# Performance work log

Hardware: AMD Instinct MI355X
Metric: run time of the kernel (lower is better)

Reference implementation:

```python
import jax, jax.numpy as jnp
import numpy as np

ALPHA = 0.2  # leaky relu slope

def setup_inputs() -> dict:
    key = jax.random.key(0)
    k1, k2, k3, k4 = jax.random.split(key, 4)
    b, n, din, dout = 8, 2048, 256, 128
    x = jax.random.normal(k1, (b, n, din), dtype=jnp.float32)
    adj = jax.random.randint(k2, (b, n, n), 0, 2, dtype=jnp.int32)
    # xavier-ish scaling for params
    W = jax.random.normal(k3, (dout, din), dtype=jnp.float32) * (1.414 * (2.0 / (din + dout)) ** 0.5)
    a = jax.random.normal(k4, (2 * dout,), dtype=jnp.float32) * (1.414 * (2.0 / (2 * dout + 1)) ** 0.5)
    return {"x": x, "adj": adj, "W": W, "a": a}

def reference(x, adj, W, a):
    # x: [b, n, din]; W: [dout, din]; a: [2*dout]
    wh = jnp.einsum('bnd,od->bno', x, W)           # [b, n, dout]
    dout = W.shape[0]
    a_src, a_dst = a[:dout], a[dout:]
    # e_ij = leaky_relu(a_src . wh_i + a_dst . wh_j)  (decomposed, avoids O(n^2 * 2d) concat)
    e = (wh @ a_src)[:, :, None] + (wh @ a_dst)[:, None, :]  # [b, n, n]
    e = jnp.where(e >= 0, e, ALPHA * e)
    e = jnp.where(adj != 0, e, -jnp.inf)
    attention = jax.nn.softmax(e, axis=2)          # [b, n, n]
    out = jnp.einsum('bij,bjo->bio', attention, wh)  # [b, n, dout]
    return jax.nn.relu(out)
```

## Files before the change

kernel.cpp:

```cpp
#include <hip/hip_runtime.h>
#include <hip/hip_bf16.h>
#include <stdint.h>

#define GAT_ALPHA 0.2f
#define LOG2E 1.4426950408889634f

typedef __attribute__((ext_vector_type(8))) __bf16 bf16x8;
typedef __attribute__((ext_vector_type(4))) float f32x4;

union B8 {
  bf16x8 b;
  unsigned short u[8];
  unsigned int w[4];
  int4 i4;
};

__device__ __forceinline__ unsigned int pk2bf(float lo, float hi) {
  union { __hip_bfloat162 h; unsigned int u; } cv;
  cv.h = __float22bfloat162_rn(make_float2(lo, hi));
  return cv.u;
}

__device__ __forceinline__ void dma16(const void* g, void* l) {
  __builtin_amdgcn_global_load_lds(
      (const __attribute__((address_space(1))) unsigned int*)g,
      (__attribute__((address_space(3))) unsigned int*)l, 16, 0, 0);
}

__global__ __launch_bounds__(256, 2) void gat_wh(
    const float* __restrict__ x, const float* __restrict__ W,
    const float* __restrict__ a, unsigned short* __restrict__ whTf,
    float* __restrict__ s_out, float* __restrict__ d_out) {
  __shared__ unsigned short WF[8][4][512];
  const int tid = threadIdx.x;
  const int wave = tid >> 6, lane = tid & 63;
  const int il = lane & 15, quad = lane >> 4;
  const int row0 = blockIdx.x * 64;
  const int i = row0 + wave * 16 + il;
  B8 av[8];
  {
    const float* xp = x + (size_t)i * 256 + quad * 8;
#pragma unroll
    for (int kc = 0; kc < 8; ++kc) {
      float4 lo = *(const float4*)(xp + kc * 32);
      float4 hi = *(const float4*)(xp + kc * 32 + 4);
      av[kc].w[0] = pk2bf(lo.x, lo.y);
      av[kc].w[1] = pk2bf(lo.z, lo.w);
      av[kc].w[2] = pk2bf(hi.x, hi.y);
      av[kc].w[3] = pk2bf(hi.z, hi.w);
    }
  }
  f32x4 acc[8];
#pragma unroll
  for (int nt = 0; nt < 8; ++nt) acc[nt] = (f32x4){0.f, 0.f, 0.f, 0.f};
#pragma unroll
  for (int h = 0; h < 2; ++h) {
    if (h) __syncthreads();
#pragma unroll
    for (int p = 0; p < 16; ++p) {
      const int f = p * 1024 + tid * 4;
      const int o = f >> 7, kk = f & 127;
      float4 v = *(const float4*)(W + o * 256 + h * 128 + kk);
      uint2 pk;
      pk.x = pk2bf(v.x, v.y);
      pk.y = pk2bf(v.z, v.w);
      *(uint2*)(&WF[o >> 4][kk >> 5][((o & 15) + (((kk & 31) >> 3) << 4)) * 8 + (kk & 7)]) = pk;
    }
    __syncthreads();
#pragma unroll
    for (int kl = 0; kl < 4; ++kl) {
      const int kc = h * 4 + kl;
#pragma unroll
      for (int nt = 0; nt < 8; ++nt) {
        B8 bv;
        bv.i4 = *(const int4*)(&WF[nt][kl][lane * 8]);
        acc[nt] = __builtin_amdgcn_mfma_f32_16x16x32_bf16(av[kc].b, bv.b, acc[nt], 0, 0, 0);
      }
    }
  }
  float asrc[8], adst[8];
#pragma unroll
  for (int nt = 0; nt < 8; ++nt) {
    asrc[nt] = a[nt * 16 + il];
    adst[nt] = a[128 + nt * 16 + il];
  }
  float sp[4], dp[4];
#pragma unroll
  for (int r = 0; r < 4; ++r) {
    float sv = 0.f, dv = 0.f;
#pragma unroll
    for (int nt = 0; nt < 8; ++nt) {
      sv += acc[nt][r] * asrc[nt];
      dv += acc[nt][r] * adst[nt];
    }
    sp[r] = sv; dp[r] = dv;
  }
#pragma unroll
  for (int off = 1; off <= 8; off <<= 1) {
#pragma unroll
    for (int r = 0; r < 4; ++r) {
      sp[r] += __shfl_xor(sp[r], off, 64);
      dp[r] += __shfl_xor(dp[r], off, 64);
    }
  }
  if (il == 0) {
#pragma unroll
    for (int r = 0; r < 4; ++r) {
      s_out[row0 + wave * 16 + quad * 4 + r] = sp[r];
      d_out[row0 + wave * 16 + quad * 4 + r] = dp[r];
    }
  }
  const int b = row0 >> 11;
  const int jc = ((row0 & 2047) >> 5) + (wave >> 1);
  const int kin = ((wave & 1) << 4) + (quad << 2);
  const int kq = kin >> 3, u0 = kin & 7;
#pragma unroll
  for (int nt = 0; nt < 8; ++nt) {
    uint2 pk;
    pk.x = pk2bf(acc[nt][0], acc[nt][1]);
    pk.y = pk2bf(acc[nt][2], acc[nt][3]);
    *(uint2*)(whTf + ((((size_t)(b * 64 + jc)) * 8 + nt) << 9) + ((il + (kq << 4)) << 3) + u0) = pk;
  }
}

#define ATTN_COMPUTE(Tval, CUR)                                                    \
  _Pragma("unroll") for (int c = 0; c < 2; ++c) {                                  \
    const int j0 = (2 * (Tval) + c) * 32;                                          \
    const unsigned int mq = (unsigned int)(mcur >> (32 * c + qo));                 \
    const float4 d0 = *(const float4*)(&dl[j0 + qo]);                              \
    const float4 d1 = *(const float4*)(&dl[j0 + qo + 4]);                          \
    const float dd[8] = {d0.x, d0.y, d0.z, d0.w, d1.x, d1.y, d1.z, d1.w};          \
    B8 af[8];                                                                      \
    _Pragma("unroll") for (int nt = 0; nt < 8; ++nt)                               \
        af[nt].i4 = *(const int4*)((const char*)&vbuf[CUR][c][nt][0] + lane * 16); \
    float pv[8];                                                                   \
    _Pragma("unroll") for (int u = 0; u < 8; ++u) {                                \
      float t0 = svL + dd[u];                                                      \
      float e2 = fmaxf(t0, GAT_ALPHA * t0);                                        \
      float p = __builtin_amdgcn_exp2f(e2);                                        \
      p = ((mq >> u) & 1u) ? p : 0.f;                                              \
      den += p;                                                                    \
      pv[u] = p;                                                                   \
    }                                                                              \
    B8 pf;                                                                         \
    pf.w[0] = pk2bf(pv[0], pv[1]);                                                 \
    pf.w[1] = pk2bf(pv[2], pv[3]);                                                 \
    pf.w[2] = pk2bf(pv[4], pv[5]);                                                 \
    pf.w[3] = pk2bf(pv[6], pv[7]);                                                 \
    _Pragma("unroll") for (int nt = 0; nt < 8; ++nt)                               \
      acc[nt] = __builtin_amdgcn_mfma_f32_16x16x32_bf16(af[nt].b, pf.b,            \
                                                        acc[nt], 0, 0, 0);         \
  }

#define ATTN_BALLOT(LVC)                                                           \
  {                                                                                \
    unsigned long long sel = __ballot(LVC[0] != 0);                                \
    _Pragma("unroll") for (int r = 1; r < 16; ++r) {                               \
      const unsigned long long mm = __ballot(LVC[r] != 0);                         \
      sel = (il == r) ? mm : sel;                                                  \
    }                                                                              \
    mcur = sel;                                                                    \
  }

#define ATTN_DMA(PAIR, NXT)                                                        \
  _Pragma("unroll") for (int h = 0; h < 2; ++h) {                                  \
    const int nt = wave * 2 + h;                                                   \
    dma16(whTb + (((size_t)(2 * (PAIR)) * 8 + nt) << 9) + (lane << 3),             \
          &vbuf[NXT][0][nt][0]);                                                   \
    dma16(whTb + (((size_t)(2 * (PAIR) + 1) * 8 + nt) << 9) + (lane << 3),         \
          &vbuf[NXT][1][nt][0]);                                                   \
  }

__global__ __launch_bounds__(256) void gat_attn(
    const int* __restrict__ adj, const unsigned short* __restrict__ whTf,
    const float* __restrict__ s, const float* __restrict__ dvec,
    float* __restrict__ out) {
  __shared__ unsigned short vbuf[2][2][8][512];
  __shared__ float dl[2048];
  const int tid = threadIdx.x;
  const int wave = tid >> 6;
  const int lane = tid & 63;
  const int il = lane & 15;
  const int quad = lane >> 4;
  const int qo = quad << 3;
  const int b = blockIdx.x & 7;
  const int tile = blockIdx.x >> 3;
  const int rbase = tile * 64;
  {
    const float* dsrc = dvec + ((size_t)b << 11);
#pragma unroll
    for (int it = 0; it < 2; ++it) {
      const int idx = it * 1024 + tid * 4;
      float4 v = *(const float4*)(dsrc + idx);
      v.x *= LOG2E; v.y *= LOG2E; v.z *= LOG2E; v.w *= LOG2E;
      *(float4*)(&dl[idx]) = v;
    }
  }
  const int* aro = adj + ((((size_t)b << 11) + rbase + wave * 16) << 11);
  int lv0[16], lvA[16], lvB[16];
#pragma unroll
  for (int r = 0; r < 16; ++r) lv0[r] = aro[(r << 11) + lane];
#pragma unroll
  for (int r = 0; r < 16; ++r) lvA[r] = aro[(r << 11) + 64 + lane];
  const unsigned short* whTb = whTf + (((size_t)b * 64) << 12);
  ATTN_DMA(0, 0);
  const int i = rbase + wave * 16 + il;
  const size_t browi = ((size_t)b << 11) + i;
  const float svL = s[browi] * LOG2E;
  f32x4 acc[8];
#pragma unroll
  for (int nt = 0; nt < 8; ++nt) acc[nt] = (f32x4){0.f, 0.f, 0.f, 0.f};
  float den = 0.f;
  unsigned long long mcur;
  ATTN_BALLOT(lv0);
  __syncthreads();

  for (int t2 = 0; t2 < 15; ++t2) {
    const int T0 = 2 * t2;
    {
      ATTN_DMA(T0 + 1, 1);
      __builtin_amdgcn_sched_barrier(0);
#pragma unroll
      for (int r = 0; r < 16; ++r) lvB[r] = aro[(r << 11) + (T0 + 2) * 64 + lane];
      ATTN_COMPUTE(T0, 0);
      ATTN_BALLOT(lvA);
      asm volatile("s_waitcnt vmcnt(16)\n\ts_barrier" ::: "memory");
    }
    {
      const int T1 = T0 + 1;
      ATTN_DMA(T1 + 1, 0);
      __builtin_amdgcn_sched_barrier(0);
#pragma unroll
      for (int r = 0; r < 16; ++r) lvA[r] = aro[(r << 11) + (T1 + 2) * 64 + lane];
      ATTN_COMPUTE(T1, 1);
      ATTN_BALLOT(lvB);
      asm volatile("s_waitcnt vmcnt(16)\n\ts_barrier" ::: "memory");
    }
  }
  {
    ATTN_DMA(31, 1);
    ATTN_COMPUTE(30, 0);
    ATTN_BALLOT(lvA);
    asm volatile("s_waitcnt vmcnt(0)\n\ts_barrier" ::: "memory");
  }
  ATTN_COMPUTE(31, 1);

  den += __shfl_xor(den, 16, 64);
  den += __shfl_xor(den, 32, 64);
  const float inv = 1.0f / den;
  float* op = out + browi * 128;
#pragma unroll
  for (int nt = 0; nt < 8; ++nt) {
    float4 v;
    v.x = fmaxf(acc[nt][0] * inv, 0.f);
    v.y = fmaxf(acc[nt][1] * inv, 0.f);
    v.z = fmaxf(acc[nt][2] * inv, 0.f);
    v.w = fmaxf(acc[nt][3] * inv, 0.f);
    *(float4*)(op + nt * 16 + quad * 4) = v;
  }
}

extern "C" void kernel_launch(void* const* d_in, const int* in_sizes, int n_in,
                              void* d_out, int out_size, void* d_ws, size_t ws_size,
                              hipStream_t stream) {
  const float* x = (const float*)d_in[0];
  const int* adj = (const int*)d_in[1];
  const float* W = (const float*)d_in[2];
  const float* a = (const float*)d_in[3];
  float* out = (float*)d_out;
  unsigned short* whTf = (unsigned short*)d_ws;
  float* s = (float*)((char*)d_ws + (size_t)4 * 1024 * 1024);
  float* dv = s + 16384;
  gat_wh<<<256, 256, 0, stream>>>(x, W, a, whTf, s, dv);
  gat_attn<<<256, 256, 0, stream>>>(adj, whTf, s, dv, out);
}
```

Baseline: 237.6 us.

## Split attention key range across wave pairs and double the grid

Each block now covers 32 rows instead of 64. Its four waves split the 2048 key columns into two halves, with each half-pair of waves handling 16 rows. The partial accumulators and denominators from the second half are reduced through shared memory before normalization and ReLU. This doubles the grid to 512 blocks and adds launch_bounds occupancy 2, aiming to use more CUs and hide adj-streaming latency. It costs a larger LDS buffer, an extra reduction and barrier, and twice as many loads of the whT tiles per row.

```diff
diff --git a/kernel.cpp b/kernel.cpp
--- a/kernel.cpp
+++ b/kernel.cpp
@@ -125,14 +125,15 @@
 
 #define ATTN_COMPUTE(Tval, CUR)                                                    \
   _Pragma("unroll") for (int c = 0; c < 2; ++c) {                                  \
-    const int j0 = (2 * (Tval) + c) * 32;                                          \
+    const int j0 = jh1024 + (2 * (Tval) + c) * 32;                                 \
     const unsigned int mq = (unsigned int)(mcur >> (32 * c + qo));                 \
     const float4 d0 = *(const float4*)(&dl[j0 + qo]);                              \
     const float4 d1 = *(const float4*)(&dl[j0 + qo + 4]);                          \
     const float dd[8] = {d0.x, d0.y, d0.z, d0.w, d1.x, d1.y, d1.z, d1.w};          \
     B8 af[8];                                                                      \
     _Pragma("unroll") for (int nt = 0; nt < 8; ++nt)                               \
-        af[nt].i4 = *(const int4*)((const char*)&vbuf[CUR][c][nt][0] + lane * 16); \
+        af[nt].i4 =                                                                \
+            *(const int4*)((const char*)&vbuf[jh][CUR][c][nt][0] + lane * 16);     \
     float pv[8];                                                                   \
     _Pragma("unroll") for (int u = 0; u < 8; ++u) {                                \
       float t0 = svL + dd[u];                                                      \
@@ -162,20 +163,17 @@
     mcur = sel;                                                                    \
   }
 
-#define ATTN_DMA(PAIR, NXT)                                                        \
-  _Pragma("unroll") for (int h = 0; h < 2; ++h) {                                  \
-    const int nt = wave * 2 + h;                                                   \
-    dma16(whTb + (((size_t)(2 * (PAIR)) * 8 + nt) << 9) + (lane << 3),             \
-          &vbuf[NXT][0][nt][0]);                                                   \
-    dma16(whTb + (((size_t)(2 * (PAIR) + 1) * 8 + nt) << 9) + (lane << 3),         \
-          &vbuf[NXT][1][nt][0]);                                                   \
-  }
-
-__global__ __launch_bounds__(256) void gat_attn(
+#define ATTN_DMA(PLOCAL, NXT)                                                      \
+  _Pragma("unroll") for (int nt = 0; nt < 8; ++nt) {                               \
+    dma16(whTb + (((size_t)((cbase + 2 * (PLOCAL)) * 8 + nt)) << 9) + (lane << 3), \
+          &vbuf[jh][NXT][rw][nt][0]);                                              \
+  }
+
+__global__ __launch_bounds__(256, 2) void gat_attn(
     const int* __restrict__ adj, const unsigned short* __restrict__ whTf,
     const float* __restrict__ s, const float* __restrict__ dvec,
     float* __restrict__ out) {
-  __shared__ unsigned short vbuf[2][2][8][512];
+  __shared__ unsigned short vbuf[2][2][2][8][512];
   __shared__ float dl[2048];
   const int tid = threadIdx.x;
   const int wave = tid >> 6;
@@ -183,9 +181,12 @@
   const int il = lane & 15;
   const int quad = lane >> 4;
   const int qo = quad << 3;
+  const int rw = wave & 1;
+  const int jh = wave >> 1;
+  const int jh1024 = jh << 10;
   const int b = blockIdx.x & 7;
   const int tile = blockIdx.x >> 3;
-  const int rbase = tile * 64;
+  const int rbase = tile * 32;
   {
     const float* dsrc = dvec + ((size_t)b << 11);
 #pragma unroll
@@ -196,15 +197,16 @@
       *(float4*)(&dl[idx]) = v;
     }
   }
-  const int* aro = adj + ((((size_t)b << 11) + rbase + wave * 16) << 11);
+  const int* aro = adj + ((((size_t)b << 11) + rbase + rw * 16) << 11) + jh1024;
   int lv0[16], lvA[16], lvB[16];
 #pragma unroll
   for (int r = 0; r < 16; ++r) lv0[r] = aro[(r << 11) + lane];
 #pragma unroll
   for (int r = 0; r < 16; ++r) lvA[r] = aro[(r << 11) + 64 + lane];
   const unsigned short* whTb = whTf + (((size_t)b * 64) << 12);
+  const int cbase = jh * 32 + rw;
   ATTN_DMA(0, 0);
-  const int i = rbase + wave * 16 + il;
+  const int i = rbase + rw * 16 + il;
   const size_t browi = ((size_t)b << 11) + i;
   const float svL = s[browi] * LOG2E;
   f32x4 acc[8];
@@ -215,7 +217,7 @@
   ATTN_BALLOT(lv0);
   __syncthreads();
 
-  for (int t2 = 0; t2 < 15; ++t2) {
+  for (int t2 = 0; t2 < 7; ++t2) {
     const int T0 = 2 * t2;
     {
       ATTN_DMA(T0 + 1, 1);
@@ -238,25 +240,44 @@
     }
   }
   {
-    ATTN_DMA(31, 1);
-    ATTN_COMPUTE(30, 0);
+    ATTN_DMA(15, 1);
+    ATTN_COMPUTE(14, 0);
     ATTN_BALLOT(lvA);
     asm volatile("s_waitcnt vmcnt(0)\n\ts_barrier" ::: "memory");
   }
-  ATTN_COMPUTE(31, 1);
-
-  den += __shfl_xor(den, 16, 64);
-  den += __shfl_xor(den, 32, 64);
-  const float inv = 1.0f / den;
-  float* op = out + browi * 128;
-#pragma unroll
-  for (int nt = 0; nt < 8; ++nt) {
-    float4 v;
-    v.x = fmaxf(acc[nt][0] * inv, 0.f);
-    v.y = fmaxf(acc[nt][1] * inv, 0.f);
-    v.z = fmaxf(acc[nt][2] * inv, 0.f);
-    v.w = fmaxf(acc[nt][3] * inv, 0.f);
-    *(float4*)(op + nt * 16 + quad * 4) = v;
+  ATTN_COMPUTE(15, 1);
+
+  __syncthreads();
+  float* mArea = (float*)vbuf;
+  if (jh == 1) {
+#pragma unroll
+    for (int nt = 0; nt < 8; ++nt)
+#pragma unroll
+      for (int r = 0; r < 4; ++r)
+        mArea[(rw * 33 + nt * 4 + r) * 64 + lane] = acc[nt][r];
+    mArea[(rw * 33 + 32) * 64 + lane] = den;
+  }
+  __syncthreads();
+  if (jh == 0) {
+#pragma unroll
+    for (int nt = 0; nt < 8; ++nt)
+#pragma unroll
+      for (int r = 0; r < 4; ++r)
+        acc[nt][r] += mArea[(rw * 33 + nt * 4 + r) * 64 + lane];
+    den += mArea[(rw * 33 + 32) * 64 + lane];
+    den += __shfl_xor(den, 16, 64);
+    den += __shfl_xor(den, 32, 64);
+    const float inv = 1.0f / den;
+    float* op = out + browi * 128;
+#pragma unroll
+    for (int nt = 0; nt < 8; ++nt) {
+      float4 v;
+      v.x = fmaxf(acc[nt][0] * inv, 0.f);
+      v.y = fmaxf(acc[nt][1] * inv, 0.f);
+      v.z = fmaxf(acc[nt][2] * inv, 0.f);
+      v.w = fmaxf(acc[nt][3] * inv, 0.f);
+      *(float4*)(op + nt * 16 + quad * 4) = v;
+    }
   }
 }
 
@@ -272,5 +293,5 @@
   float* s = (float*)((char*)d_ws + (size_t)4 * 1024 * 1024);
   float* dv = s + 16384;
   gat_wh<<<256, 256, 0, stream>>>(x, W, a, whTf, s, dv);
-  gat_attn<<<256, 256, 0, stream>>>(adj, whTf, s, dv, out);
-}
+  gat_attn<<<512, 256, 0, stream>>>(adj, whTf, s, dv, out);
+}
```

Measured after the change: 237.6 us. No clear change (+0.0%).
